# Kernel optimization log

Hardware: AMD Instinct MI355X
Metric: run time of the kernel (lower is better)

Reference implementation:

```python
import jax, jax.numpy as jnp
import numpy as np
from jax import lax

N, M, T, IN, H, DEPTH = 64, 10, 160, 40, 256, 3
B = N * M
EPS = 1e-8


def setup_inputs() -> dict:
    key = jax.random.key(0)
    ks = jax.random.split(key, 20)
    s = 1.0 / np.sqrt(H)  # torch LSTM init scale
    inp = {
        "sequences": jax.random.normal(ks[0], (B, T, IN), jnp.float32),
        "len_sequences": jax.random.randint(ks[1], (B,), 80, T + 1, jnp.int32),
        "w_sim": jnp.float32(0.5),
        "b_sim": jnp.float32(0.5),
    }
    in_sizes = [IN, H, H]
    for l in range(DEPTH):
        k = 2 + 4 * l
        inp[f"Wih{l}"] = jax.random.uniform(ks[k], (4 * H, in_sizes[l]), jnp.float32, -s, s)
        inp[f"Whh{l}"] = jax.random.uniform(ks[k + 1], (4 * H, H), jnp.float32, -s, s)
        inp[f"bih{l}"] = jax.random.uniform(ks[k + 2], (4 * H,), jnp.float32, -s, s)
        inp[f"bhh{l}"] = jax.random.uniform(ks[k + 3], (4 * H,), jnp.float32, -s, s)
    return inp


def _lstm_layer(x_tbf, mask_tb, Wih, Whh, bih, bhh):
    """x_tbf: [T,B,F] time-major. mask_tb: [T,B] valid-step mask.
    Returns (h_seq [T,B,H], c_last [B,H]) where c_last is the cell state at
    the last valid timestep of each sequence (packed-sequence semantics)."""
    b = x_tbf.shape[1]
    h0 = jnp.zeros((b, H), x_tbf.dtype)
    c0 = jnp.zeros((b, H), x_tbf.dtype)

    def step(carry, xm):
        h, c = carry
        xt, mt = xm
        g = xt @ Wih.T + bih + h @ Whh.T + bhh  # [B,4H]
        i, f, gg, o = jnp.split(g, 4, axis=1)
        cn = jax.nn.sigmoid(f) * c + jax.nn.sigmoid(i) * jnp.tanh(gg)
        hn = jax.nn.sigmoid(o) * jnp.tanh(cn)
        m = mt[:, None]
        h2 = jnp.where(m, hn, h)
        c2 = jnp.where(m, cn, c)
        return (h2, c2), h2

    (hT, cT), h_seq = lax.scan(step, (h0, c0), (x_tbf, mask_tb))
    return h_seq, cT


def reference(sequences, len_sequences, Wih0, Whh0, bih0, bhh0,
              Wih1, Whh1, bih1, bhh1, Wih2, Whh2, bih2, bhh2,
              w_sim, b_sim):
    lens = len_sequences.astype(jnp.int32)
    x = jnp.transpose(sequences, (1, 0, 2))  # [T,B,IN]
    mask = jnp.arange(T)[:, None] < lens[None, :]  # [T,B]

    layers = [(Wih0, Whh0, bih0, bhh0), (Wih1, Whh1, bih1, bhh1), (Wih2, Whh2, bih2, bhh2)]
    c_last = None
    for (Wih, Whh, bih, bhh) in layers:
        x, c_last = _lstm_layer(x, mask, Wih, Whh, bih, bhh)
    E = c_last  # [B,H] final-layer cell state per utterance (original order)

    # L2-normalize embeddings (F.normalize, p=2, dim=1)
    E = E / jnp.maximum(jnp.linalg.norm(E, axis=1, keepdims=True), 1e-12)

    Er = E.reshape(N, M, H)
    C = Er.mean(axis=1)  # [N,H] speaker centroids
    # exclusive centroids exactly as source: (M*c_j + E_i)/(M-1)
    Cm = ((M * C[:, None, :] + Er) / (M - 1)).reshape(B, H)

    En = E / jnp.maximum(jnp.linalg.norm(E, axis=1, keepdims=True), EPS)
    Cn = C / jnp.maximum(jnp.linalg.norm(C, axis=1, keepdims=True), EPS)
    Cmn = Cm / jnp.maximum(jnp.linalg.norm(Cm, axis=1, keepdims=True), EPS)

    S = (En @ Cn.T) * w_sim + b_sim  # [B,N]: cos(E_i, c_j)*w + b

    # diagonal block: row i, col i//M uses exclusive centroid
    d = jnp.sum(En * Cmn, axis=1)  # [B]
    rows = jnp.arange(B)
    cols = jnp.repeat(jnp.arange(N), M)
    S = S.at[rows, cols].set(d * w_sim + b_sim)
    return S


if __name__ == "__main__":
    out = reference(**setup_inputs())
    print(out.shape, out.dtype)
```

## Files before the change

### kernel.cpp

```cpp
#include <hip/hip_runtime.h>
#include <cstdint>
#include <cstddef>

typedef __attribute__((ext_vector_type(8))) short short8;
typedef __attribute__((ext_vector_type(4))) float f32x4;
typedef __attribute__((ext_vector_type(4))) unsigned short us4;

#define N_SPK 64
#define M_UTT 10
#define T_SEQ 160
#define IN_F  40
#define H_DIM 256
#define B_TOT 640
#define G4    1024
#define FSTR  64

__device__ __forceinline__ unsigned short f2bf(float f) {
  unsigned int u = __float_as_uint(f);
  u += 0x7FFFu + ((u >> 16) & 1u);
  return (unsigned short)(u >> 16);
}
__device__ __forceinline__ float b2f(unsigned short u) {
  return __uint_as_float(((unsigned int)u) << 16);
}
__device__ __forceinline__ float sigm(float x) {
  return 1.f / (1.f + __expf(-x));
}
__device__ __forceinline__ float tanh_fast(float x) {
  return 1.f - 2.f / (1.f + __expf(2.f * x));
}
__device__ __forceinline__ unsigned long long ato_ld(const unsigned long long* p) {
  return __hip_atomic_load(p, __ATOMIC_RELAXED, __HIP_MEMORY_SCOPE_AGENT);
}
__device__ __forceinline__ void ato_st(unsigned long long* p, unsigned long long v) {
  __hip_atomic_store(p, v, __ATOMIC_RELAXED, __HIP_MEMORY_SCOPE_AGENT);
}
__device__ __forceinline__ int flg_ld(const int* p) {
  return __hip_atomic_load(p, __ATOMIC_RELAXED, __HIP_MEMORY_SCOPE_AGENT);
}
__device__ __forceinline__ void flg_st(int* p, int v) {
  __hip_atomic_store(p, v, __ATOMIC_RELAXED, __HIP_MEMORY_SCOPE_AGENT);
}

#define LDS_BARRIER() do {                                      \
  asm volatile("s_waitcnt lgkmcnt(0)" ::: "memory");            \
  __builtin_amdgcn_s_barrier();                                 \
  asm volatile("" ::: "memory");                                \
} while (0)

__global__ void pack_w_kernel(const float* __restrict__ W, short* __restrict__ out,
                              int Kin, int Ktiles) {
  int idx = blockIdx.x * 256 + threadIdx.x;
  int total = 64 * Ktiles * 64;
  if (idx >= total) return;
  int lane = idx & 63;
  int rest = idx >> 6;
  int ks   = rest % Ktiles;
  int tile = rest / Ktiles;
  int n  = tile * 16 + (lane & 15);
  int k0 = ks * 32 + (lane >> 4) * 8;
  short8 v;
#pragma unroll
  for (int j = 0; j < 8; ++j) {
    int k = k0 + j;
    float f = (k < Kin) ? W[(size_t)n * Kin + k] : 0.f;
    v[j] = (short)f2bf(f);
  }
  *(short8*)&out[(size_t)idx * 8] = v;
}

__global__ void bias_sum_kernel(const float* __restrict__ a, const float* __restrict__ b,
                                float* __restrict__ o) {
  int i = blockIdx.x * 256 + threadIdx.x;
  if (i < G4) o[i] = a[i] + b[i];
}

__global__ __launch_bounds__(256, 2)
void gate_gemm0(const float* __restrict__ seq, const short* __restrict__ Wp,
                const float* __restrict__ bias, unsigned short* __restrict__ G) {
  const int btile = blockIdx.x % 40;
  const int rest  = blockIdx.x / 40;
  const int tg    = rest & 3;
  const int chunk = rest >> 2;
  const int tid = threadIdx.x, lane = tid & 63, wave = tid >> 6;
  const int nl = lane & 15, mq = lane >> 4;

  for (int mg = 0; mg < 4; ++mg) {
    const int t0 = chunk * 16 + mg * 4;
    f32x4 acc[4][4];
#pragma unroll
    for (int q = 0; q < 4; ++q) {
      int tile = tg * 16 + wave + 4 * q;
      float bv = bias[tile * 16 + nl];
#pragma unroll
      for (int mm = 0; mm < 4; ++mm) acc[mm][q] = (f32x4){bv, bv, bv, bv};
    }
    for (int kt = 0; kt < 2; ++kt) {
      short8 a[4];
      const int m = btile * 16 + nl;
      const int k0 = kt * 32 + mq * 8;
#pragma unroll
      for (int mm = 0; mm < 4; ++mm) {
#pragma unroll
        for (int j = 0; j < 8; ++j) {
          int k = k0 + j;
          float f = (k < IN_F) ? seq[((size_t)m * T_SEQ + (t0 + mm)) * IN_F + k] : 0.f;
          a[mm][j] = (short)f2bf(f);
        }
      }
#pragma unroll
      for (int q = 0; q < 4; ++q) {
        int tile = tg * 16 + wave + 4 * q;
        short8 b = *(const short8*)&Wp[(((size_t)tile * 2 + kt) * 64 + lane) * 8];
#pragma unroll
        for (int mm = 0; mm < 4; ++mm)
          acc[mm][q] = __builtin_amdgcn_mfma_f32_16x16x32_bf16(a[mm], b, acc[mm][q], 0, 0, 0);
      }
    }
#pragma unroll
    for (int mm = 0; mm < 4; ++mm)
#pragma unroll
      for (int q = 0; q < 4; ++q) {
        int tile = tg * 16 + wave + 4 * q;
        us4 o;
#pragma unroll
        for (int r = 0; r < 4; ++r) o[r] = f2bf(acc[mm][q][r]);
        *(us4*)&G[(((size_t)(t0 + mm) * 40 + btile) * 64 + tile) * 256 + lane * 4] = o;
      }
  }
}

template<int L>
__device__ __forceinline__ void rec_stage(
    int S, int hb,
    const short* __restrict__ Whhp, const short* __restrict__ Wihp,
    const unsigned short* __restrict__ G0, const float* __restrict__ biasl,
    unsigned long long* __restrict__ hxch, int* __restrict__ flags,
    const int* __restrict__ lens, float* __restrict__ c_state,
    unsigned short* h_sh, unsigned short* x_sh,
    float* bias_sh, short* wih_lds, int* len_sh)
{
  const int tid = threadIdx.x, lane = tid & 63, wave = tid >> 6;
  const int mq = lane >> 4, nl = lane & 15;
  const int lc = wave * 16 + nl;
  const int colown = hb * 64 + lc;
  unsigned long long* x64 = (unsigned long long*)x_sh;

  short8 wregH[4][8];
#pragma unroll
  for (int g = 0; g < 4; ++g) {
    const int tile = g * 16 + hb * 4 + wave;
#pragma unroll
    for (int s = 0; s < 8; ++s) {
      const int ktp = (2 * hb + s) & 7;
      wregH[g][s] = *(const short8*)&Whhp[(((size_t)tile * 8 + ktp) * 64 + lane) * 8];
    }
  }
  short8 wregI[4][4];
  if (L >= 1) {
#pragma unroll
    for (int g = 0; g < 4; ++g) {
      const int tile = g * 16 + hb * 4 + wave;
#pragma unroll
      for (int kt = 0; kt < 4; ++kt)
        wregI[g][kt] = *(const short8*)&Wihp[(((size_t)tile * 8 + kt) * 64 + lane) * 8];
    }
    for (int i = tid; i < 4096; i += 256) {
      int tl = i >> 6, ln = i & 63;
      int lt = tl >> 2, kt4 = tl & 3;
      int gt = (lt >> 2) * 16 + hb * 4 + (lt & 3);
      *(short8*)&wih_lds[(lt * 4 + kt4) * 512 + ln * 8] =
          *(const short8*)&Wihp[(((size_t)gt * 8 + 4 + kt4) * 64 + ln) * 8];
    }
    for (int i = tid; i < 1024; i += 256) bias_sh[i] = biasl[i];
  }
  for (int i = tid; i < 64 * 264; i += 256) h_sh[i] = 0;
  if (tid < 64) len_sh[tid] = lens[S * 64 + tid];

  float creg[16];
#pragma unroll
  for (int i = 0; i < 16; ++i) creg[i] = 0.f;

  if (L == 0) {
    us4 tmp[16];
#pragma unroll
    for (int m = 0; m < 4; ++m)
#pragma unroll
      for (int g = 0; g < 4; ++g) {
        const int tile = g * 16 + hb * 4 + wave;
        tmp[m * 4 + g] = *(const us4*)&G0[(((size_t)0 * 40 + S * 4 + m) * 64 + tile) * 256 + lane * 4];
      }
#pragma unroll
    for (int u = 0; u < 16; ++u)
      x64[u * 256 + tid] = *(unsigned long long*)&tmp[u];
  }
  __syncthreads();

  const int fself = L * 40 + S * 4 + hb;

  unsigned long long xr[16];
  if (L >= 1) {
    if (tid < 4)
      while (flg_ld(&flags[((L - 1) * 40 + S * 4 + tid) * FSTR]) < 1) {}
    __syncthreads();
    const unsigned long long* xb0 =
        hxch + ((size_t)((0 * 3 + (L - 1)) * 10 + S)) * 4096;
#pragma unroll
    for (int u = 0; u < 16; ++u) xr[u] = ato_ld(&xb0[u * 256 + tid]);
  }
  unsigned long long pr[12];

  for (int t = 0; t < T_SEQ; ++t) {
    const int par = t & 3;

    if (L < 2 && tid < 4)
      while (flg_ld(&flags[((L + 1) * 40 + S * 4 + tid) * FSTR]) < t - 3) {}

    f32x4 acc[4][4];
    if (L == 0) {
#pragma unroll
      for (int m = 0; m < 4; ++m)
#pragma unroll
        for (int g = 0; g < 4; ++g) {
          unsigned long long v = x64[(m * 4 + g) * 256 + tid];
          us4 gv = *(us4*)&v;
#pragma unroll
          for (int r = 0; r < 4; ++r) acc[m][g][r] = b2f(gv[r]);
        }
    } else {
#pragma unroll
      for (int g = 0; g < 4; ++g) {
        const int tile = g * 16 + hb * 4 + wave;
        float bv = bias_sh[tile * 16 + nl];
#pragma unroll
        for (int m = 0; m < 4; ++m) acc[m][g] = (f32x4){bv, bv, bv, bv};
      }
    }
#pragma unroll
    for (int s = 0; s < 2; ++s) {
      const int ktp = (2 * hb + s) & 7;
      short8 a[4];
#pragma unroll
      for (int m = 0; m < 4; ++m)
        a[m] = *(const short8*)&h_sh[(m * 16 + nl) * 264 + ktp * 32 + mq * 8];
#pragma unroll
      for (int m = 0; m < 4; ++m)
#pragma unroll
        for (int g = 0; g < 4; ++g)
          acc[m][g] = __builtin_amdgcn_mfma_f32_16x16x32_bf16(a[m], wregH[g][s], acc[m][g], 0, 0, 0);
    }
    if (L >= 1) {
#pragma unroll
      for (int u = 0; u < 16; ++u) {
        int j = u * 256 + tid, pp = j >> 10, jj = j & 1023;
        *(unsigned long long*)&x_sh[(jj >> 4) * 264 + pp * 64 + (jj & 15) * 4] = xr[u];
      }
      LDS_BARRIER();
#pragma unroll
      for (int kt = 0; kt < 8; ++kt) {
        short8 a[4];
#pragma unroll
        for (int m = 0; m < 4; ++m)
          a[m] = *(const short8*)&x_sh[(m * 16 + nl) * 264 + kt * 32 + mq * 8];
#pragma unroll
        for (int g = 0; g < 4; ++g) {
          short8 b = (kt < 4) ? wregI[g][kt]
                              : *(const short8*)&wih_lds[((g * 4 + wave) * 4 + (kt - 4)) * 512 + lane * 8];
#pragma unroll
          for (int m = 0; m < 4; ++m)
            acc[m][g] = __builtin_amdgcn_mfma_f32_16x16x32_bf16(a[m], b, acc[m][g], 0, 0, 0);
        }
      }
    }
    if (t > 0) {
#pragma unroll
      for (int u = 0; u < 12; ++u) {
        int j = u * 256 + tid;
        int pp = j >> 10, jj = j & 1023;
        int p = pp + (pp >= hb ? 1 : 0);
        *(unsigned long long*)&h_sh[(jj >> 4) * 264 + p * 64 + (jj & 15) * 4] = pr[u];
      }
    }
    __syncthreads();
#pragma unroll
    for (int s = 2; s < 8; ++s) {
      const int ktp = (2 * hb + s) & 7;
      short8 a[4];
#pragma unroll
      for (int m = 0; m < 4; ++m)
        a[m] = *(const short8*)&h_sh[(m * 16 + nl) * 264 + ktp * 32 + mq * 8];
#pragma unroll
      for (int m = 0; m < 4; ++m)
#pragma unroll
        for (int g = 0; g < 4; ++g)
          acc[m][g] = __builtin_amdgcn_mfma_f32_16x16x32_bf16(a[m], wregH[g][s], acc[m][g], 0, 0, 0);
    }
    unsigned short hv[16];
#pragma unroll
    for (int m = 0; m < 4; ++m)
#pragma unroll
      for (int r = 0; r < 4; ++r) {
        const int row = m * 16 + mq * 4 + r;
        float c_old = creg[m * 4 + r];
        float cn = sigm(acc[m][1][r]) * c_old + sigm(acc[m][0][r]) * tanh_fast(acc[m][2][r]);
        float hn = sigm(acc[m][3][r]) * tanh_fast(cn);
        bool upd = t < len_sh[row];
        if (upd) creg[m * 4 + r] = cn;
        hv[m * 4 + r] = upd ? f2bf(hn) : h_sh[row * 264 + colown];
      }
    __syncthreads();
#pragma unroll
    for (int m = 0; m < 4; ++m)
#pragma unroll
      for (int r = 0; r < 4; ++r)
        h_sh[(m * 16 + mq * 4 + r) * 264 + colown] = hv[m * 4 + r];
    __syncthreads();
    unsigned long long* myslab =
        hxch + ((size_t)((par * 3 + L) * 10 + S) * 4 + hb) * 1024;
    for (int j = tid; j < 1024; j += 256) {
      int sample = j >> 4, l4 = j & 15;
      unsigned long long v =
          *(const unsigned long long*)&h_sh[sample * 264 + hb * 64 + l4 * 4];
      ato_st(&myslab[j], v);
    }
    __syncthreads();
    if (tid == 0) flg_st(&flags[fself * FSTR], t + 1);
    if (L == 0) {
      int tn = (t + 1 < T_SEQ) ? t + 1 : t;
      us4 tmp[16];
#pragma unroll
      for (int m = 0; m < 4; ++m)
#pragma unroll
        for (int g = 0; g < 4; ++g) {
          const int tile = g * 16 + hb * 4 + wave;
          tmp[m * 4 + g] = *(const us4*)&G0[(((size_t)tn * 40 + S * 4 + m) * 64 + tile) * 256 + lane * 4];
        }
#pragma unroll
      for (int u = 0; u < 16; ++u)
        x64[u * 256 + tid] = *(unsigned long long*)&tmp[u];
    }
    if (t + 1 < T_SEQ) {
      if (tid < 3) {
        int p = tid + (tid >= hb ? 1 : 0);
        while (flg_ld(&flags[(L * 40 + S * 4 + p) * FSTR]) < t + 1) {}
      }
      if (L >= 1 && tid >= 64 && tid < 68)
        while (flg_ld(&flags[((L - 1) * 40 + S * 4 + (tid - 64)) * FSTR]) < t + 2) {}
      __syncthreads();
      if (L >= 1) {
        const unsigned long long* xb =
            hxch + ((size_t)((((t + 1) & 3) * 3 + (L - 1)) * 10 + S)) * 4096;
#pragma unroll
        for (int u = 0; u < 16; ++u) xr[u] = ato_ld(&xb[u * 256 + tid]);
      }
#pragma unroll
      for (int u = 0; u < 12; ++u) {
        int j = u * 256 + tid;
        int pp = j >> 10, jj = j & 1023;
        int p = pp + (pp >= hb ? 1 : 0);
        pr[u] = ato_ld(&hxch[((size_t)((par * 3 + L) * 10 + S) * 4 + p) * 1024 + jj]);
      }
    }
  }
  if (L == 2) {
#pragma unroll
    for (int m = 0; m < 4; ++m)
#pragma unroll
      for (int r = 0; r < 4; ++r) {
        const int row = m * 16 + mq * 4 + r;
        c_state[((size_t)S * 64 + row) * 256 + colown] = creg[m * 4 + r];
      }
  }
}

__global__ __launch_bounds__(256, 1)
void fused_lstm(const short* __restrict__ Whhp_all, const short* __restrict__ Wih1p,
                const short* __restrict__ Wih2p, const float* __restrict__ biasc,
                const unsigned short* __restrict__ G0, const int* __restrict__ lens,
                unsigned long long* __restrict__ hxch, int* __restrict__ flags,
                float* __restrict__ c_state)
{
  __shared__ unsigned short h_sh[64 * 264];
  __shared__ unsigned short x_sh[64 * 264];
  __shared__ float bias_sh[1024];
  __shared__ short wih_lds[16 * 4 * 512];
  __shared__ int len_sh[64];

  const int bid  = blockIdx.x;
  const int xcd  = bid & 7;
  const int j    = bid >> 3;
  const int g    = (j >> 2) * 8 + xcd;
  if (g >= 30) return;
  const int L  = g / 10;
  const int S  = g % 10;
  const int hb = j & 3;

  if (L == 0)
    rec_stage<0>(S, hb, Whhp_all,          nullptr, G0, nullptr,
                 hxch, flags, lens, c_state, h_sh, x_sh, bias_sh, wih_lds, len_sh);
  else if (L == 1)
    rec_stage<1>(S, hb, Whhp_all + 262144, Wih1p, G0, biasc + G4,
                 hxch, flags, lens, c_state, h_sh, x_sh, bias_sh, wih_lds, len_sh);
  else
    rec_stage<2>(S, hb, Whhp_all + 524288, Wih2p, G0, biasc + 2 * G4,
                 hxch, flags, lens, c_state, h_sh, x_sh, bias_sh, wih_lds, len_sh);
}

__global__ void k_norm(const float* __restrict__ E, float* __restrict__ E1,
                       float* __restrict__ En) {
  int row  = blockIdx.x * 4 + (threadIdx.x >> 6);
  int lane = threadIdx.x & 63;
  const float* e = E + (size_t)row * H_DIM;
  float v[4]; float ss = 0.f;
#pragma unroll
  for (int j = 0; j < 4; ++j) { v[j] = e[lane + 64 * j]; ss += v[j] * v[j]; }
#pragma unroll
  for (int m = 32; m >= 1; m >>= 1) ss += __shfl_xor(ss, m, 64);
  float nrm  = sqrtf(ss);
  float inv1 = 1.f / fmaxf(nrm, 1e-12f);
  float inv2 = 1.f / fmaxf(nrm * inv1, 1e-8f);
#pragma unroll
  for (int j = 0; j < 4; ++j) {
    float e1 = v[j] * inv1;
    E1[(size_t)row * H_DIM + lane + 64 * j] = e1;
    En[(size_t)row * H_DIM + lane + 64 * j] = e1 * inv2;
  }
}

__global__ void k_cent(const float* __restrict__ E1, float* __restrict__ C,
                       float* __restrict__ CnT) {
  int n = blockIdx.x;
  int lane = threadIdx.x;
  float v[4]; float ss = 0.f;
#pragma unroll
  for (int j = 0; j < 4; ++j) {
    int col = lane + 64 * j;
    float s = 0.f;
    for (int m = 0; m < M_UTT; ++m) s += E1[((size_t)n * M_UTT + m) * H_DIM + col];
    v[j] = s / (float)M_UTT;
    ss += v[j] * v[j];
  }
#pragma unroll
  for (int m = 32; m >= 1; m >>= 1) ss += __shfl_xor(ss, m, 64);
  float inv = 1.f / fmaxf(sqrtf(ss), 1e-8f);
#pragma unroll
  for (int j = 0; j < 4; ++j) {
    int col = lane + 64 * j;
    C[(size_t)n * H_DIM + col]  = v[j];
    CnT[(size_t)col * N_SPK + n] = v[j] * inv;
  }
}

__global__ void k_cm(const float* __restrict__ E1, const float* __restrict__ C,
                     float* __restrict__ Cmn) {
  int b    = blockIdx.x * 4 + (threadIdx.x >> 6);
  int lane = threadIdx.x & 63;
  int spk  = b / M_UTT;
  float v[4]; float ss = 0.f;
#pragma unroll
  for (int j = 0; j < 4; ++j) {
    int col = lane + 64 * j;
    v[j] = ((float)M_UTT * C[(size_t)spk * H_DIM + col] + E1[(size_t)b * H_DIM + col])
           / (float)(M_UTT - 1);
    ss += v[j] * v[j];
  }
#pragma unroll
  for (int m = 32; m >= 1; m >>= 1) ss += __shfl_xor(ss, m, 64);
  float inv = 1.f / fmaxf(sqrtf(ss), 1e-8f);
#pragma unroll
  for (int j = 0; j < 4; ++j)
    Cmn[(size_t)b * H_DIM + lane + 64 * j] = v[j] * inv;
}

__global__ void k_sim(const float* __restrict__ En, const float* __restrict__ CnT,
                      const float* __restrict__ Cmn, const float* __restrict__ w_sim,
                      const float* __restrict__ b_sim, float* __restrict__ S) {
  int b = blockIdx.x;
  int n = threadIdx.x;
  int diag = b / M_UTT;
  float w = w_sim[0], bb = b_sim[0];
  float s = 0.f;
  for (int k = 0; k < H_DIM; ++k) {
    float en = En[(size_t)b * H_DIM + k];
    float c  = (n == diag) ? Cmn[(size_t)b * H_DIM + k] : CnT[(size_t)k * N_SPK + n];
    s += en * c;
  }
  S[(size_t)b * N_SPK + n] = s * w + bb;
}

#define O_WHH   0ull
#define O_WIH0  1572864ull
#define O_WIH1  1703936ull
#define O_WIH2  2228224ull
#define O_BIAS  2752512ull
#define O_CST   2764800ull
#define O_E1    3420160ull
#define O_EN    4075520ull
#define O_C     4730880ull
#define O_CNT   4796416ull
#define O_CMN   4861952ull
#define O_FLG   5517312ull
#define O_HXCH  5548032ull
#define O_G0    9480192ull

extern "C" void kernel_launch(void* const* d_in, const int* in_sizes, int n_in,
                              void* d_out, int out_size, void* d_ws, size_t ws_size,
                              hipStream_t stream) {
  const float* seq   = (const float*)d_in[0];
  const int*   lens  = (const int*)d_in[1];
  const float* w_sim = (const float*)d_in[2];
  const float* b_sim = (const float*)d_in[3];
  const float* Wih[3] = {(const float*)d_in[4],  (const float*)d_in[8],  (const float*)d_in[12]};
  const float* Whh[3] = {(const float*)d_in[5],  (const float*)d_in[9],  (const float*)d_in[13]};
  const float* bih[3] = {(const float*)d_in[6],  (const float*)d_in[10], (const float*)d_in[14]};
  const float* bhh[3] = {(const float*)d_in[7],  (const float*)d_in[11], (const float*)d_in[15]};

  char* ws = (char*)d_ws;
  short* Whhp_all = (short*)(ws + O_WHH);
  short* Wihp[3] = {(short*)(ws + O_WIH0), (short*)(ws + O_WIH1), (short*)(ws + O_WIH2)};
  float* biasc = (float*)(ws + O_BIAS);
  float* c_state = (float*)(ws + O_CST);
  float* E1  = (float*)(ws + O_E1);
  float* En  = (float*)(ws + O_EN);
  float* C   = (float*)(ws + O_C);
  float* CnT = (float*)(ws + O_CNT);
  float* Cmn = (float*)(ws + O_CMN);
  int* flags = (int*)(ws + O_FLG);
  unsigned long long* hxch = (unsigned long long*)(ws + O_HXCH);
  unsigned short* G0 = (unsigned short*)(ws + O_G0);
  float* S = (float*)d_out;

  pack_w_kernel<<<32, 256, 0, stream>>>(Wih[0], Wihp[0], IN_F, 2);
  pack_w_kernel<<<128, 256, 0, stream>>>(Whh[0], Whhp_all, H_DIM, 8);
  pack_w_kernel<<<128, 256, 0, stream>>>(Whh[1], Whhp_all + 262144, H_DIM, 8);
  pack_w_kernel<<<128, 256, 0, stream>>>(Whh[2], Whhp_all + 524288, H_DIM, 8);
  pack_w_kernel<<<128, 256, 0, stream>>>(Wih[1], Wihp[1], H_DIM, 8);
  pack_w_kernel<<<128, 256, 0, stream>>>(Wih[2], Wihp[2], H_DIM, 8);
  for (int l = 0; l < 3; ++l)
    bias_sum_kernel<<<4, 256, 0, stream>>>(bih[l], bhh[l], biasc + l * G4);

  gate_gemm0<<<1600, 256, 0, stream>>>(seq, Wihp[0], biasc, G0);

  (void)hipMemsetAsync(ws + O_FLG, 0, 30720, stream);
  fused_lstm<<<128, 256, 0, stream>>>(Whhp_all, Wihp[1], Wihp[2], biasc, G0, lens,
                                      hxch, flags, c_state);

  k_norm<<<160, 256, 0, stream>>>(c_state, E1, En);
  k_cent<<<N_SPK, 64, 0, stream>>>(E1, C, CnT);
  k_cm<<<160, 256, 0, stream>>>(E1, C, Cmn);
  k_sim<<<B_TOT, 64, 0, stream>>>(En, CnT, Cmn, w_sim, b_sim, S);
}
```

Before: 1.663 ms.

## Specialize recurrent stage on hidden block and restructure layer-0 h exchange

Makes the hidden-block index a template parameter so index arithmetic becomes compile-time constants. For layer 0, the peer h slices are loaded and written to LDS at the end of the step, then one barrier runs and all 8 k-tiles of the recurrent matmul are done without a mid-step split. Deeper layers keep the overlap where the own-slice k-tiles are computed before peer data arrives. The LDS barrier macro now uses a scheduling barrier, which limits instruction reordering around it, and the template expansion increases code size.

```diff
diff --git a/kernel.cpp b/kernel.cpp
--- a/kernel.cpp
+++ b/kernel.cpp
@@ -45,7 +45,7 @@
 #define LDS_BARRIER() do {                                      \
   asm volatile("s_waitcnt lgkmcnt(0)" ::: "memory");            \
   __builtin_amdgcn_s_barrier();                                 \
-  asm volatile("" ::: "memory");                                \
+  __builtin_amdgcn_sched_barrier(0);                            \
 } while (0)
 
 __global__ void pack_w_kernel(const float* __restrict__ W, short* __restrict__ out,
@@ -130,9 +130,9 @@
   }
 }
 
-template<int L>
+template<int L, int HB>
 __device__ __forceinline__ void rec_stage(
-    int S, int hb,
+    int S,
     const short* __restrict__ Whhp, const short* __restrict__ Wihp,
     const unsigned short* __restrict__ G0, const float* __restrict__ biasl,
     unsigned long long* __restrict__ hxch, int* __restrict__ flags,
@@ -143,16 +143,16 @@
   const int tid = threadIdx.x, lane = tid & 63, wave = tid >> 6;
   const int mq = lane >> 4, nl = lane & 15;
   const int lc = wave * 16 + nl;
-  const int colown = hb * 64 + lc;
+  const int colown = HB * 64 + lc;
   unsigned long long* x64 = (unsigned long long*)x_sh;
 
   short8 wregH[4][8];
 #pragma unroll
   for (int g = 0; g < 4; ++g) {
-    const int tile = g * 16 + hb * 4 + wave;
+    const int tile = g * 16 + HB * 4 + wave;
 #pragma unroll
     for (int s = 0; s < 8; ++s) {
-      const int ktp = (2 * hb + s) & 7;
+      const int ktp = (L == 0) ? s : ((2 * HB + s) & 7);
       wregH[g][s] = *(const short8*)&Whhp[(((size_t)tile * 8 + ktp) * 64 + lane) * 8];
     }
   }
@@ -160,7 +160,7 @@
   if (L >= 1) {
 #pragma unroll
     for (int g = 0; g < 4; ++g) {
-      const int tile = g * 16 + hb * 4 + wave;
+      const int tile = g * 16 + HB * 4 + wave;
 #pragma unroll
       for (int kt = 0; kt < 4; ++kt)
         wregI[g][kt] = *(const short8*)&Wihp[(((size_t)tile * 8 + kt) * 64 + lane) * 8];
@@ -168,7 +168,7 @@
     for (int i = tid; i < 4096; i += 256) {
       int tl = i >> 6, ln = i & 63;
       int lt = tl >> 2, kt4 = tl & 3;
-      int gt = (lt >> 2) * 16 + hb * 4 + (lt & 3);
+      int gt = (lt >> 2) * 16 + HB * 4 + (lt & 3);
       *(short8*)&wih_lds[(lt * 4 + kt4) * 512 + ln * 8] =
           *(const short8*)&Wihp[(((size_t)gt * 8 + 4 + kt4) * 64 + ln) * 8];
     }
@@ -187,7 +187,7 @@
     for (int m = 0; m < 4; ++m)
 #pragma unroll
       for (int g = 0; g < 4; ++g) {
-        const int tile = g * 16 + hb * 4 + wave;
+        const int tile = g * 16 + HB * 4 + wave;
         tmp[m * 4 + g] = *(const us4*)&G0[(((size_t)0 * 40 + S * 4 + m) * 64 + tile) * 256 + lane * 4];
       }
 #pragma unroll
@@ -196,7 +196,7 @@
   }
   __syncthreads();
 
-  const int fself = L * 40 + S * 4 + hb;
+  const int fself = L * 40 + S * 4 + HB;
 
   unsigned long long xr[16];
   if (L >= 1) {
@@ -227,29 +227,39 @@
 #pragma unroll
           for (int r = 0; r < 4; ++r) acc[m][g][r] = b2f(gv[r]);
         }
+#pragma unroll
+      for (int kt = 0; kt < 8; ++kt) {
+        short8 a[4];
+#pragma unroll
+        for (int m = 0; m < 4; ++m)
+          a[m] = *(const short8*)&h_sh[(m * 16 + nl) * 264 + kt * 32 + mq * 8];
+#pragma unroll
+        for (int m = 0; m < 4; ++m)
+#pragma unroll
+          for (int g = 0; g < 4; ++g)
+            acc[m][g] = __builtin_amdgcn_mfma_f32_16x16x32_bf16(a[m], wregH[g][kt], acc[m][g], 0, 0, 0);
+      }
     } else {
 #pragma unroll
       for (int g = 0; g < 4; ++g) {
-        const int tile = g * 16 + hb * 4 + wave;
+        const int tile = g * 16 + HB * 4 + wave;
         float bv = bias_sh[tile * 16 + nl];
 #pragma unroll
         for (int m = 0; m < 4; ++m) acc[m][g] = (f32x4){bv, bv, bv, bv};
       }
-    }
-#pragma unroll
-    for (int s = 0; s < 2; ++s) {
-      const int ktp = (2 * hb + s) & 7;
-      short8 a[4];
-#pragma unroll
-      for (int m = 0; m < 4; ++m)
-        a[m] = *(const short8*)&h_sh[(m * 16 + nl) * 264 + ktp * 32 + mq * 8];
-#pragma unroll
-      for (int m = 0; m < 4; ++m)
-#pragma unroll
-        for (int g = 0; g < 4; ++g)
-          acc[m][g] = __builtin_amdgcn_mfma_f32_16x16x32_bf16(a[m], wregH[g][s], acc[m][g], 0, 0, 0);
-    }
-    if (L >= 1) {
+#pragma unroll
+      for (int s = 0; s < 2; ++s) {
+        const int ktp = (2 * HB + s) & 7;
+        short8 a[4];
+#pragma unroll
+        for (int m = 0; m < 4; ++m)
+          a[m] = *(const short8*)&h_sh[(m * 16 + nl) * 264 + ktp * 32 + mq * 8];
+#pragma unroll
+        for (int m = 0; m < 4; ++m)
+#pragma unroll
+          for (int g = 0; g < 4; ++g)
+            acc[m][g] = __builtin_amdgcn_mfma_f32_16x16x32_bf16(a[m], wregH[g][s], acc[m][g], 0, 0, 0);
+      }
 #pragma unroll
       for (int u = 0; u < 16; ++u) {
         int j = u * 256 + tid, pp = j >> 10, jj = j & 1023;
@@ -271,29 +281,29 @@
             acc[m][g] = __builtin_amdgcn_mfma_f32_16x16x32_bf16(a[m], b, acc[m][g], 0, 0, 0);
         }
       }
-    }
-    if (t > 0) {
-#pragma unroll
-      for (int u = 0; u < 12; ++u) {
-        int j = u * 256 + tid;
-        int pp = j >> 10, jj = j & 1023;
-        int p = pp + (pp >= hb ? 1 : 0);
-        *(unsigned long long*)&h_sh[(jj >> 4) * 264 + p * 64 + (jj & 15) * 4] = pr[u];
-      }
-    }
-    __syncthreads();
-#pragma unroll
-    for (int s = 2; s < 8; ++s) {
-      const int ktp = (2 * hb + s) & 7;
-      short8 a[4];
-#pragma unroll
-      for (int m = 0; m < 4; ++m)
-        a[m] = *(const short8*)&h_sh[(m * 16 + nl) * 264 + ktp * 32 + mq * 8];
-#pragma unroll
-      for (int m = 0; m < 4; ++m)
-#pragma unroll
-        for (int g = 0; g < 4; ++g)
-          acc[m][g] = __builtin_amdgcn_mfma_f32_16x16x32_bf16(a[m], wregH[g][s], acc[m][g], 0, 0, 0);
+      if (t > 0) {
+#pragma unroll
+        for (int u = 0; u < 12; ++u) {
+          int j = u * 256 + tid;
+          int pp = j >> 10, jj = j & 1023;
+          int p = pp + (pp >= HB ? 1 : 0);
+          *(unsigned long long*)&h_sh[(jj >> 4) * 264 + p * 64 + (jj & 15) * 4] = pr[u];
+        }
+      }
+      __syncthreads();
+#pragma unroll
+      for (int s = 2; s < 8; ++s) {
+        const int ktp = (2 * HB + s) & 7;
+        short8 a[4];
+#pragma unroll
+        for (int m = 0; m < 4; ++m)
+          a[m] = *(const short8*)&h_sh[(m * 16 + nl) * 264 + ktp * 32 + mq * 8];
+#pragma unroll
+        for (int m = 0; m < 4; ++m)
+#pragma unroll
+          for (int g = 0; g < 4; ++g)
+            acc[m][g] = __builtin_amdgcn_mfma_f32_16x16x32_bf16(a[m], wregH[g][s], acc[m][g], 0, 0, 0);
+      }
     }
     unsigned short hv[16];
 #pragma unroll
@@ -316,11 +326,11 @@
         h_sh[(m * 16 + mq * 4 + r) * 264 + colown] = hv[m * 4 + r];
     __syncthreads();
     unsigned long long* myslab =
-        hxch + ((size_t)((par * 3 + L) * 10 + S) * 4 + hb) * 1024;
+        hxch + ((size_t)((par * 3 + L) * 10 + S) * 4 + HB) * 1024;
     for (int j = tid; j < 1024; j += 256) {
       int sample = j >> 4, l4 = j & 15;
       unsigned long long v =
-          *(const unsigned long long*)&h_sh[sample * 264 + hb * 64 + l4 * 4];
+          *(const unsigned long long*)&h_sh[sample * 264 + HB * 64 + l4 * 4];
       ato_st(&myslab[j], v);
     }
     __syncthreads();
@@ -332,7 +342,7 @@
       for (int m = 0; m < 4; ++m)
 #pragma unroll
         for (int g = 0; g < 4; ++g) {
-          const int tile = g * 16 + hb * 4 + wave;
+          const int tile = g * 16 + HB * 4 + wave;
           tmp[m * 4 + g] = *(const us4*)&G0[(((size_t)tn * 40 + S * 4 + m) * 64 + tile) * 256 + lane * 4];
         }
 #pragma unroll
@@ -341,7 +351,7 @@
     }
     if (t + 1 < T_SEQ) {
       if (tid < 3) {
-        int p = tid + (tid >= hb ? 1 : 0);
+        int p = tid + (tid >= HB ? 1 : 0);
         while (flg_ld(&flags[(L * 40 + S * 4 + p) * FSTR]) < t + 1) {}
       }
       if (L >= 1 && tid >= 64 && tid < 68)
@@ -352,13 +362,30 @@
             hxch + ((size_t)((((t + 1) & 3) * 3 + (L - 1)) * 10 + S)) * 4096;
 #pragma unroll
         for (int u = 0; u < 16; ++u) xr[u] = ato_ld(&xb[u * 256 + tid]);
-      }
-#pragma unroll
-      for (int u = 0; u < 12; ++u) {
-        int j = u * 256 + tid;
-        int pp = j >> 10, jj = j & 1023;
-        int p = pp + (pp >= hb ? 1 : 0);
-        pr[u] = ato_ld(&hxch[((size_t)((par * 3 + L) * 10 + S) * 4 + p) * 1024 + jj]);
+#pragma unroll
+        for (int u = 0; u < 12; ++u) {
+          int j = u * 256 + tid;
+          int pp = j >> 10, jj = j & 1023;
+          int p = pp + (pp >= HB ? 1 : 0);
+          pr[u] = ato_ld(&hxch[((size_t)((par * 3 + L) * 10 + S) * 4 + p) * 1024 + jj]);
+        }
+      } else {
+        unsigned long long prl[12];
+#pragma unroll
+        for (int u = 0; u < 12; ++u) {
+          int j = u * 256 + tid;
+          int pp = j >> 10, jj = j & 1023;
+          int p = pp + (pp >= HB ? 1 : 0);
+          prl[u] = ato_ld(&hxch[((size_t)((par * 3 + L) * 10 + S) * 4 + p) * 1024 + jj]);
+        }
+#pragma unroll
+        for (int u = 0; u < 12; ++u) {
+          int j = u * 256 + tid;
+          int pp = j >> 10, jj = j & 1023;
+          int p = pp + (pp >= HB ? 1 : 0);
+          *(unsigned long long*)&h_sh[(jj >> 4) * 264 + p * 64 + (jj & 15) * 4] = prl[u];
+        }
+        __syncthreads();
       }
     }
   }
@@ -395,15 +422,22 @@
   const int S  = g % 10;
   const int hb = j & 3;
 
-  if (L == 0)
-    rec_stage<0>(S, hb, Whhp_all,          nullptr, G0, nullptr,
-                 hxch, flags, lens, c_state, h_sh, x_sh, bias_sh, wih_lds, len_sh);
-  else if (L == 1)
-    rec_stage<1>(S, hb, Whhp_all + 262144, Wih1p, G0, biasc + G4,
-                 hxch, flags, lens, c_state, h_sh, x_sh, bias_sh, wih_lds, len_sh);
-  else
-    rec_stage<2>(S, hb, Whhp_all + 524288, Wih2p, G0, biasc + 2 * G4,
-                 hxch, flags, lens, c_state, h_sh, x_sh, bias_sh, wih_lds, len_sh);
+#define DISPATCH(LL, OFF, WIH, BIAS)                                          \
+  do {                                                                        \
+    if (hb == 0)      rec_stage<LL, 0>(S, Whhp_all + OFF, WIH, G0, BIAS,      \
+        hxch, flags, lens, c_state, h_sh, x_sh, bias_sh, wih_lds, len_sh);    \
+    else if (hb == 1) rec_stage<LL, 1>(S, Whhp_all + OFF, WIH, G0, BIAS,      \
+        hxch, flags, lens, c_state, h_sh, x_sh, bias_sh, wih_lds, len_sh);    \
+    else if (hb == 2) rec_stage<LL, 2>(S, Whhp_all + OFF, WIH, G0, BIAS,      \
+        hxch, flags, lens, c_state, h_sh, x_sh, bias_sh, wih_lds, len_sh);    \
+    else              rec_stage<LL, 3>(S, Whhp_all + OFF, WIH, G0, BIAS,      \
+        hxch, flags, lens, c_state, h_sh, x_sh, bias_sh, wih_lds, len_sh);    \
+  } while (0)
+
+  if (L == 0)      DISPATCH(0, 0,      (const short*)nullptr, (const float*)nullptr);
+  else if (L == 1) DISPATCH(1, 262144, Wih1p, biasc + G4);
+  else             DISPATCH(2, 524288, Wih2p, biasc + 2 * G4);
+#undef DISPATCH
 }
 
 __global__ void k_norm(const float* __restrict__ E, float* __restrict__ E1,
```

After: 1.680 ms. About the same (+1.0%).
